# Kernel optimization log

Measured on AMD Instinct MI355X. Metric: run time of the kernel, lower is better.

The kernel has to match this reference:

```python
import jax, jax.numpy as jnp
import numpy as np

B, T, DIM = 2, 2048, 1024
N_HEADS, HEAD_DIM, WINDOW = 16, 64, 512
EPS = 0.01


def _rmsnorm(x, gamma, eps):
    # x: [B, T, H*D] float32; normalize over last dim
    rms = jnp.sqrt(jnp.mean(jnp.square(x), axis=-1, keepdims=True) + eps)
    return x / rms * gamma


def setup_inputs() -> dict:
    key = jax.random.key(0)
    ks = jax.random.split(key, 5)
    s = 1.0 / np.sqrt(DIM)
    return {
        "x": jax.random.normal(ks[0], (B, T, DIM), jnp.float32),
        "wq": jax.random.normal(ks[1], (N_HEADS * HEAD_DIM, DIM), jnp.float32) * s,
        "wk": jax.random.normal(ks[2], (N_HEADS * HEAD_DIM, DIM), jnp.float32) * s,
        "wv": jax.random.normal(ks[3], (N_HEADS * HEAD_DIM, DIM), jnp.float32) * s,
        "wo": jax.random.normal(ks[4], (DIM, N_HEADS * HEAD_DIM), jnp.float32) * s,
        "q_gamma": jnp.ones((N_HEADS * HEAD_DIM,), jnp.float32),
        "k_gamma": jnp.ones((N_HEADS * HEAD_DIM,), jnp.float32),
    }


def reference(x, wq, wk, wv, wo, q_gamma, k_gamma):
    Bx, Tx, _ = x.shape
    H, D = N_HEADS, HEAD_DIM
    # projections (Linear with weight [out,in]): [B,T,H*D]
    q = x @ wq.T
    k = x @ wk.T
    v = (x @ wv.T).reshape(Bx, Tx, H, D).transpose(0, 2, 1, 3)  # [B,H,T,D]
    # QK RMSNorm over the flattened H*D dimension (float32 math)
    q = _rmsnorm(q, q_gamma, 1e-6).reshape(Bx, Tx, H, D).transpose(0, 2, 1, 3)
    k = _rmsnorm(k, k_gamma, 1e-6).reshape(Bx, Tx, H, D).transpose(0, 2, 1, 3)
    scale = 1.0 / np.sqrt(D)
    scores = jnp.einsum("bhqd,bhkd->bhqk", q, k) * scale  # [B,H,T,T]
    # ALiBi bias: slopes[h] * (j - i)
    slopes = jnp.asarray([2.0 ** (-8.0 / H * (h + 1)) for h in range(H)], jnp.float32)
    pos = jnp.arange(Tx)
    dist = (pos[None, :] - pos[:, None]).astype(jnp.float32)  # [T,T], dist[i,j]=j-i
    scores = scores + slopes[None, :, None, None] * dist[None, None]
    # causal (j>i) OR beyond sliding window (i-j > window_size)
    j_minus_i = pos[None, :] - pos[:, None]
    mask = (j_minus_i > 0) | (j_minus_i < -WINDOW)
    scores = jnp.where(mask[None, None], -1e9, scores)
    attn = jax.nn.softmax(scores, axis=-1)
    out = jnp.einsum("bhqk,bhkd->bhqd", attn, v)  # [B,H,T,D]
    out = out.transpose(0, 2, 1, 3).reshape(Bx, Tx, H * D)
    return out @ wo.T
```

## Files before the change

### kernel.cpp

```cpp
#include <hip/hip_runtime.h>
#include <stdint.h>

typedef unsigned short u16;
typedef __bf16 bf16x8 __attribute__((ext_vector_type(8)));
typedef float f32x4 __attribute__((ext_vector_type(4)));

#define MFMA16(a, b, c) __builtin_amdgcn_mfma_f32_16x16x32_bf16((a), (b), (c), 0, 0, 0)

__device__ __forceinline__ u16 f2bf(float f) {
  union { float f; uint32_t u; } v; v.f = f;
  uint32_t r = v.u + 0x7fffu + ((v.u >> 16) & 1u);
  return (u16)(r >> 16);
}
__device__ __forceinline__ float bf2f(u16 h) {
  union { uint32_t u; float f; } v; v.u = ((uint32_t)h) << 16;
  return v.f;
}
__device__ __forceinline__ void gload_lds16(const void* g, void* l) {
  __builtin_amdgcn_global_load_lds(
      (const __attribute__((address_space(1))) uint32_t*)(uintptr_t)g,
      (__attribute__((address_space(3))) uint32_t*)(uintptr_t)l, 16, 0, 0);
}
__device__ __forceinline__ uint32_t cvt_pk_bf16(float a, float b) {
  uint32_t r;
  asm("v_cvt_pk_bf16_f32 %0, %1, %2" : "=v"(r) : "v"(a), "v"(b));
  return r;
}

__global__ void k_cvt_all(const float* __restrict__ x, const float* __restrict__ wq,
                          const float* __restrict__ wk, const float* __restrict__ wv,
                          const float* __restrict__ wo, u16* __restrict__ xb,
                          u16* __restrict__ wqb, u16* __restrict__ wkb, u16* __restrict__ wvb,
                          u16* __restrict__ wob) {
  const int i = blockIdx.x * 256 + threadIdx.x;
  const float* src; u16* dst; int off;
  if (i < 1048576)      { src = x;  dst = xb;  off = i; }
  else if (i < 1310720) { src = wq; dst = wqb; off = i - 1048576; }
  else if (i < 1572864) { src = wk; dst = wkb; off = i - 1310720; }
  else if (i < 1835008) { src = wv; dst = wvb; off = i - 1572864; }
  else                  { src = wo; dst = wob; off = i - 1835008; }
  const float4 v = ((const float4*)src)[off];
  u16 o[4] = { f2bf(v.x), f2bf(v.y), f2bf(v.z), f2bf(v.w) };
  *(uint2*)(dst + 4 * (size_t)off) = *(const uint2*)o;
}

template <bool BF16_OUT>
__device__ __forceinline__ void gemm_core(const u16* __restrict__ A, const u16* __restrict__ Bw,
                                          void* __restrict__ C) {
  constexpr int K = 1024, N = 1024, NT = K / 32;
  __shared__ __align__(16) u16 As[2][128 * 32];
  __shared__ __align__(16) u16 Bs[2][128 * 32];
  const int tid = threadIdx.x, l = tid & 63, w = tid >> 6;
  const int wm = (w >> 1) * 64, wn = (w & 1) * 64;
  const int tn = blockIdx.x * 128, tm = blockIdx.y * 128;
  const int lo = l & 15, hi8 = (l >> 4) * 8;
  f32x4 acc[4][4] = {};

  const int srow = l >> 2, scol = (l & 3) * 8;
  const int c0 = w * 2, c1 = w * 2 + 1;
  const u16* Ag0 = A + (size_t)(tm + c0 * 16 + srow) * K + scol;
  const u16* Ag1 = A + (size_t)(tm + c1 * 16 + srow) * K + scol;
  const u16* Bg0 = Bw + (size_t)(tn + c0 * 16 + srow) * K + scol;
  const u16* Bg1 = Bw + (size_t)(tn + c1 * 16 + srow) * K + scol;

#define STAGE_G(t, buf)                           \
  {                                               \
    const int kt_ = (t) * 32;                     \
    gload_lds16(Ag0 + kt_, &As[(buf)][c0 * 512]); \
    gload_lds16(Ag1 + kt_, &As[(buf)][c1 * 512]); \
    gload_lds16(Bg0 + kt_, &Bs[(buf)][c0 * 512]); \
    gload_lds16(Bg1 + kt_, &Bs[(buf)][c1 * 512]); \
  }

  STAGE_G(0, 0);
  STAGE_G(1, 1);

  for (int t = 0; t < NT; ++t) {
    const int cur = t & 1;
    if (t + 1 < NT) {
      asm volatile("s_waitcnt vmcnt(4)");
    } else {
      asm volatile("s_waitcnt vmcnt(0)");
    }
    __builtin_amdgcn_s_barrier();
    __builtin_amdgcn_sched_barrier(0);

    bf16x8 af[4], bfr[4];
#pragma unroll
    for (int m = 0; m < 4; ++m) af[m] = *(const bf16x8*)&As[cur][(wm + m * 16 + lo) * 32 + hi8];
#pragma unroll
    for (int n = 0; n < 4; ++n) bfr[n] = *(const bf16x8*)&Bs[cur][(wn + n * 16 + lo) * 32 + hi8];
#pragma unroll
    for (int m = 0; m < 4; ++m)
#pragma unroll
      for (int n = 0; n < 4; ++n) acc[m][n] = MFMA16(af[m], bfr[n], acc[m][n]);

    __builtin_amdgcn_sched_barrier(0);
    __builtin_amdgcn_s_barrier();
    __builtin_amdgcn_sched_barrier(0);
    if (t + 2 < NT) STAGE_G(t + 2, cur);
  }
#undef STAGE_G

  const int r0 = (l >> 4) * 4;
#pragma unroll
  for (int m = 0; m < 4; ++m)
#pragma unroll
    for (int n = 0; n < 4; ++n)
#pragma unroll
      for (int r = 0; r < 4; ++r) {
        const size_t idx = (size_t)(tm + wm + m * 16 + r0 + r) * N + (tn + wn + n * 16 + lo);
        if (BF16_OUT) ((u16*)C)[idx] = f2bf(acc[m][n][r]);
        else ((float*)C)[idx] = acc[m][n][r];
      }
}

__global__ __launch_bounds__(256, 3) void k_gemm_qkv(
    const u16* __restrict__ X, const u16* __restrict__ Wq, const u16* __restrict__ Wk,
    const u16* __restrict__ Wv, u16* __restrict__ Q, u16* __restrict__ Kt, u16* __restrict__ V) {
  const u16* B = blockIdx.z == 0 ? Wq : blockIdx.z == 1 ? Wk : Wv;
  u16* C = blockIdx.z == 0 ? Q : blockIdx.z == 1 ? Kt : V;
  gemm_core<true>(X, B, C);
}
__global__ __launch_bounds__(256, 3) void k_gemm_out(const u16* __restrict__ Ao,
                                                     const u16* __restrict__ Wo,
                                                     float* __restrict__ C) {
  gemm_core<false>(Ao, Wo, C);
}

__global__ __launch_bounds__(256) void k_rmsnorm(u16* __restrict__ Q, u16* __restrict__ Kt,
                                                 const float* __restrict__ qg,
                                                 const float* __restrict__ kg) {
  const int row = blockIdx.x;
  u16* base = (row < 4096) ? (Q + (size_t)row * 1024) : (Kt + (size_t)(row - 4096) * 1024);
  const float* g = (row < 4096) ? qg : kg;
  const int tid = threadIdx.x;
  ushort4 v = ((const ushort4*)base)[tid];
  float f0 = bf2f(v.x), f1 = bf2f(v.y), f2 = bf2f(v.z), f3 = bf2f(v.w);
  float ss = f0 * f0 + f1 * f1 + f2 * f2 + f3 * f3;
#pragma unroll
  for (int off = 32; off >= 1; off >>= 1) ss += __shfl_xor(ss, off, 64);
  __shared__ float wsum[4];
  if ((tid & 63) == 0) wsum[tid >> 6] = ss;
  __syncthreads();
  ss = wsum[0] + wsum[1] + wsum[2] + wsum[3];
  const float rinv = rsqrtf(ss * (1.0f / 1024.0f) + 1e-6f);
  const float4 gv = ((const float4*)g)[tid];
  v.x = f2bf(f0 * rinv * gv.x);
  v.y = f2bf(f1 * rinv * gv.y);
  v.z = f2bf(f2 * rinv * gv.z);
  v.w = f2bf(f3 * rinv * gv.w);
  ((ushort4*)base)[tid] = v;
}

__global__ __launch_bounds__(512, 4) void k_attn(const u16* __restrict__ Q,
                                                 const u16* __restrict__ Kt,
                                                 const u16* __restrict__ V,
                                                 u16* __restrict__ O) {
  constexpr int T = 2048, HD = 1024, WIN = 512;
  const int nlin = blockIdx.x + (blockIdx.y << 4) + (blockIdx.z << 8);
  const int wid = (nlin & 7) * 64 + (nlin >> 3);
  const int qb = (wid & 15) * 128, h = (wid >> 4) & 15, b = wid >> 8;
  const int tid = threadIdx.x, l = tid & 63, w = tid >> 6;
  const int lo = l & 15, hi = l >> 4;
  const int qw = qb + w * 16;
  const int qg = qw + lo;

  __shared__ __align__(16) u16 Ks[2][64 * 64];
  __shared__ __align__(16) u16 Vt[2][64 * 72];

  const size_t bT = (size_t)b * T;

  bf16x8 qf[2];
  {
    const u16* Qr = Q + (bT + qw + lo) * HD + h * 64 + hi * 8;
    qf[0] = *(const bf16x8*)(Qr);
    qf[1] = *(const bf16x8*)(Qr + 32);
  }

  const int srow = tid >> 3;
  const int kcol = 8 * ((tid & 7) ^ (srow & 7));
  const int vkv = 2 * (l & 31) + (l >> 5);
  const int vd0 = w * 8;
  const u16* Kg0 = Kt + bT * HD + h * 64;
  const u16* Vg0 = V + bT * HD + h * 64;

  float m_r = -1e30f, l_r = 0.f;
  f32x4 o_acc[4] = {};

  const float L2E = 1.4426950408889634f;
  const float scaleL = 0.125f * L2E;
  const float slopeL = exp2f(-0.5f * (float)(h + 1)) * L2E;
  float cn[4], cr[4];
#pragma unroll
  for (int n = 0; n < 4; ++n) cn[n] = slopeL * (float)(n * 16);
#pragma unroll
  for (int r = 0; r < 4; ++r) cr[r] = slopeL * (float)r;

  const int kvs = (qb >= WIN) ? (qb - WIN) : 0;
  const int nt = (qb + 128 - kvs) >> 6;

  {
    const uint4 pkt = *(const uint4*)(Vg0 + (size_t)(kvs + vkv) * HD + vd0);
    gload_lds16(Kg0 + (size_t)(kvs + srow) * HD + kcol, &Ks[0][tid * 8]);
    const u16* e = (const u16*)&pkt;
#pragma unroll
    for (int j = 0; j < 8; ++j) Vt[0][(vd0 + j) * 72 + vkv] = e[j];
  }
  asm volatile("s_waitcnt vmcnt(0)");
  asm volatile("s_waitcnt lgkmcnt(0)");
  __builtin_amdgcn_s_barrier();
  __builtin_amdgcn_sched_barrier(0);

  for (int t = 0; t < nt; ++t) {
    const int kv0 = kvs + t * 64, cur = t & 1;
    const bool pf_next = (t + 1 < nt);
    uint4 vnext;
    if (pf_next) {
      vnext = *(const uint4*)(Vg0 + (size_t)(kv0 + 64 + vkv) * HD + vd0);
      gload_lds16(Kg0 + (size_t)(kv0 + 64 + srow) * HD + kcol, &Ks[cur ^ 1][tid * 8]);
      asm volatile("s_waitcnt vmcnt(2)");
    } else {
      asm volatile("s_waitcnt vmcnt(0)");
    }
    __builtin_amdgcn_s_barrier();
    __builtin_amdgcn_sched_barrier(0);

    const bool active = (kv0 <= qw + 15) && (kv0 + 63 + WIN >= qw);
    if (active) {
      f32x4 st[4];
      __builtin_amdgcn_s_setprio(1);
#pragma unroll
      for (int n = 0; n < 4; ++n) {
        f32x4 z = {0.f, 0.f, 0.f, 0.f};
        const int row = n * 16 + lo;
        const int swz = (row & 7) << 4;
#pragma unroll
        for (int kk = 0; kk < 2; ++kk) {
          const bf16x8 kf =
              *(const bf16x8*)((const char*)Ks[cur] + row * 128 + ((kk * 64 + hi * 16) ^ swz));
          z = MFMA16(kf, qf[kk], z);
        }
        st[n] = z;
      }
      __builtin_amdgcn_s_setprio(0);

      const int ddb = kv0 + hi * 4 - qg;
      const float bb = slopeL * (float)ddb;
      float bn[4];
#pragma unroll
      for (int n = 0; n < 4; ++n) bn[n] = bb + cn[n];
      const bool interior = (kv0 + 63 <= qw) && (qw + 15 - kv0 <= WIN);
      if (interior) {
#pragma unroll
        for (int n = 0; n < 4; ++n)
#pragma unroll
          for (int r = 0; r < 4; ++r) st[n][r] = st[n][r] * scaleL + (bn[n] + cr[r]);
      } else {
#pragma unroll
        for (int n = 0; n < 4; ++n)
#pragma unroll
          for (int r = 0; r < 4; ++r) {
            const int dd = ddb + n * 16 + r;
            const float s_ = st[n][r] * scaleL + (bn[n] + cr[r]);
            st[n][r] = (dd > 0 || dd < -WIN) ? -1e30f : s_;
          }
      }

      float mx = -1e30f;
#pragma unroll
      for (int n = 0; n < 4; ++n) {
        const float a = fmaxf(st[n][0], st[n][1]), c = fmaxf(st[n][2], st[n][3]);
        mx = fmaxf(mx, fmaxf(a, c));
      }
      mx = fmaxf(mx, __shfl_xor(mx, 16, 64));
      mx = fmaxf(mx, __shfl_xor(mx, 32, 64));
      const float mn = fmaxf(m_r, mx);
      const float alpha = exp2f(m_r - mn);
      m_r = mn;

      float rs = 0.f;
#pragma unroll
      for (int n = 0; n < 4; ++n)
#pragma unroll
        for (int r = 0; r < 4; ++r) {
          const float p = exp2f(st[n][r] - mn);
          st[n][r] = p;
          rs += p;
        }
      rs += __shfl_xor(rs, 16, 64);
      rs += __shfl_xor(rs, 32, 64);
      l_r = l_r * alpha + rs;
#pragma unroll
      for (int nd = 0; nd < 4; ++nd)
#pragma unroll
        for (int r = 0; r < 4; ++r) o_acc[nd][r] *= alpha;

      uint32_t pk[4][2];
#pragma unroll
      for (int n = 0; n < 4; ++n)
#pragma unroll
        for (int d = 0; d < 2; ++d) pk[n][d] = cvt_pk_bf16(st[n][2 * d], st[n][2 * d + 1]);

      uint32_t pfr[2][4];
#pragma unroll
      for (int kk = 0; kk < 2; ++kk)
#pragma unroll
        for (int d = 0; d < 2; ++d) {
          auto s1 = __builtin_amdgcn_permlane32_swap(pk[kk * 2][d], pk[kk * 2 + 1][d], false, false);
          auto s2 = __builtin_amdgcn_permlane16_swap(s1[0], s1[1], false, false);
          pfr[kk][d] = s2[0];
          pfr[kk][2 + d] = s2[1];
        }

      __builtin_amdgcn_s_setprio(1);
#pragma unroll
      for (int kk = 0; kk < 2; ++kk) {
        union { uint32_t u[4]; bf16x8 v; } pu;
#pragma unroll
        for (int d2 = 0; d2 < 4; ++d2) pu.u[d2] = pfr[kk][d2];
        const bf16x8 pv = pu.v;
#pragma unroll
        for (int nd = 0; nd < 4; ++nd) {
          const bf16x8 vf = *(const bf16x8*)&Vt[cur][(nd * 16 + lo) * 72 + kk * 32 + hi * 8];
          o_acc[nd] = MFMA16(vf, pv, o_acc[nd]);
        }
      }
      __builtin_amdgcn_s_setprio(0);
    }

    if (pf_next) {
      const u16* e = (const u16*)&vnext;
#pragma unroll
      for (int j = 0; j < 8; ++j) Vt[cur ^ 1][(vd0 + j) * 72 + vkv] = e[j];
    }
    __builtin_amdgcn_sched_barrier(0);
    asm volatile("s_waitcnt lgkmcnt(0)");
    __builtin_amdgcn_s_barrier();
    __builtin_amdgcn_sched_barrier(0);
  }

  const float inv = 1.f / l_r;
  u16* Og = O + (bT + qw + lo) * HD + h * 64;
#pragma unroll
  for (int nd = 0; nd < 4; ++nd) {
    uint2 pack;
    pack.x = cvt_pk_bf16(o_acc[nd][0] * inv, o_acc[nd][1] * inv);
    pack.y = cvt_pk_bf16(o_acc[nd][2] * inv, o_acc[nd][3] * inv);
    *(uint2*)(Og + nd * 16 + hi * 4) = pack;
  }
}

extern "C" void kernel_launch(void* const* d_in, const int* in_sizes, int n_in,
                              void* d_out, int out_size, void* d_ws, size_t ws_size,
                              hipStream_t stream) {
  const float* x = (const float*)d_in[0];
  const float* wq = (const float*)d_in[1];
  const float* wk = (const float*)d_in[2];
  const float* wv = (const float*)d_in[3];
  const float* wo = (const float*)d_in[4];
  const float* qg = (const float*)d_in[5];
  const float* kg = (const float*)d_in[6];
  float* out = (float*)d_out;

  char* ws = (char*)d_ws;
  const size_t MB = (size_t)1 << 20;
  u16* xb  = (u16*)(ws + 0 * MB);
  u16* wqb = (u16*)(ws + 8 * MB);
  u16* wkb = (u16*)(ws + 10 * MB);
  u16* wvb = (u16*)(ws + 12 * MB);
  u16* wob = (u16*)(ws + 14 * MB);
  u16* qb  = (u16*)(ws + 16 * MB);
  u16* kb  = (u16*)(ws + 24 * MB);
  u16* vb  = (u16*)(ws + 32 * MB);
  u16* ab  = xb;

  k_cvt_all<<<8192, 256, 0, stream>>>(x, wq, wk, wv, wo, xb, wqb, wkb, wvb, wob);
  k_gemm_qkv<<<dim3(8, 32, 3), 256, 0, stream>>>(xb, wqb, wkb, wvb, qb, kb, vb);
  k_rmsnorm<<<8192, 256, 0, stream>>>(qb, kb, qg, kg);
  k_attn<<<dim3(16, 16, 2), 512, 0, stream>>>(qb, kb, vb, ab);
  k_gemm_out<<<dim3(8, 32, 1), 256, 0, stream>>>(ab, wob, out);
}
```

Before: 106.3 us.

## Process 128-key tiles per attention iteration with single-buffered transposed V

Doubles the KV tile from 64 to 128 keys per loop iteration, halving the number of iterations and barrier pairs and the online-softmax rescale overhead. K stays double-buffered via async global-to-LDS loads. V becomes a single LDS buffer written after a barrier, with the global V loads issued early into registers. This adds register pressure (st[8], pk[8][2]) and means more masked work on window edges, and the V stage now waits on all outstanding loads at the end of each iteration, which may expose latency.

```diff
diff --git a/kernel.cpp b/kernel.cpp
--- a/kernel.cpp
+++ b/kernel.cpp
@@ -166,8 +166,8 @@
   const int qw = qb + w * 16;
   const int qg = qw + lo;
 
-  __shared__ __align__(16) u16 Ks[2][64 * 64];
-  __shared__ __align__(16) u16 Vt[2][64 * 72];
+  __shared__ __align__(16) u16 Ks[2][128 * 64];
+  __shared__ __align__(16) u16 Vt[64 * 136];
 
   const size_t bT = (size_t)b * T;
 
@@ -191,47 +191,50 @@
   const float L2E = 1.4426950408889634f;
   const float scaleL = 0.125f * L2E;
   const float slopeL = exp2f(-0.5f * (float)(h + 1)) * L2E;
-  float cn[4], cr[4];
-#pragma unroll
-  for (int n = 0; n < 4; ++n) cn[n] = slopeL * (float)(n * 16);
+  float cn[8], cr[4];
+#pragma unroll
+  for (int n = 0; n < 8; ++n) cn[n] = slopeL * (float)(n * 16);
 #pragma unroll
   for (int r = 0; r < 4; ++r) cr[r] = slopeL * (float)r;
 
   const int kvs = (qb >= WIN) ? (qb - WIN) : 0;
-  const int nt = (qb + 128 - kvs) >> 6;
+  const int nt = (qb + 128 - kvs) >> 7;
 
   {
-    const uint4 pkt = *(const uint4*)(Vg0 + (size_t)(kvs + vkv) * HD + vd0);
     gload_lds16(Kg0 + (size_t)(kvs + srow) * HD + kcol, &Ks[0][tid * 8]);
-    const u16* e = (const u16*)&pkt;
-#pragma unroll
-    for (int j = 0; j < 8; ++j) Vt[0][(vd0 + j) * 72 + vkv] = e[j];
-  }
-  asm volatile("s_waitcnt vmcnt(0)");
+    gload_lds16(Kg0 + (size_t)(kvs + 64 + srow) * HD + kcol, &Ks[0][64 * 64 + tid * 8]);
+    const uint4 p0 = *(const uint4*)(Vg0 + (size_t)(kvs + vkv) * HD + vd0);
+    const uint4 p1 = *(const uint4*)(Vg0 + (size_t)(kvs + 64 + vkv) * HD + vd0);
+    asm volatile("s_waitcnt vmcnt(0)");
+    const u16* e0 = (const u16*)&p0;
+    const u16* e1 = (const u16*)&p1;
+#pragma unroll
+    for (int j = 0; j < 8; ++j) {
+      Vt[(vd0 + j) * 136 + vkv] = e0[j];
+      Vt[(vd0 + j) * 136 + 64 + vkv] = e1[j];
+    }
+  }
   asm volatile("s_waitcnt lgkmcnt(0)");
   __builtin_amdgcn_s_barrier();
   __builtin_amdgcn_sched_barrier(0);
 
   for (int t = 0; t < nt; ++t) {
-    const int kv0 = kvs + t * 64, cur = t & 1;
+    const int kv0 = kvs + t * 128, cur = t & 1;
     const bool pf_next = (t + 1 < nt);
-    uint4 vnext;
+    uint4 vn0, vn1;
     if (pf_next) {
-      vnext = *(const uint4*)(Vg0 + (size_t)(kv0 + 64 + vkv) * HD + vd0);
-      gload_lds16(Kg0 + (size_t)(kv0 + 64 + srow) * HD + kcol, &Ks[cur ^ 1][tid * 8]);
-      asm volatile("s_waitcnt vmcnt(2)");
-    } else {
-      asm volatile("s_waitcnt vmcnt(0)");
-    }
-    __builtin_amdgcn_s_barrier();
-    __builtin_amdgcn_sched_barrier(0);
-
-    const bool active = (kv0 <= qw + 15) && (kv0 + 63 + WIN >= qw);
+      gload_lds16(Kg0 + (size_t)(kv0 + 128 + srow) * HD + kcol, &Ks[cur ^ 1][tid * 8]);
+      gload_lds16(Kg0 + (size_t)(kv0 + 192 + srow) * HD + kcol, &Ks[cur ^ 1][64 * 64 + tid * 8]);
+      vn0 = *(const uint4*)(Vg0 + (size_t)(kv0 + 128 + vkv) * HD + vd0);
+      vn1 = *(const uint4*)(Vg0 + (size_t)(kv0 + 192 + vkv) * HD + vd0);
+    }
+
+    const bool active = (kv0 <= qw + 15) && (kv0 + 127 + WIN >= qw);
     if (active) {
-      f32x4 st[4];
+      f32x4 st[8];
       __builtin_amdgcn_s_setprio(1);
 #pragma unroll
-      for (int n = 0; n < 4; ++n) {
+      for (int n = 0; n < 8; ++n) {
         f32x4 z = {0.f, 0.f, 0.f, 0.f};
         const int row = n * 16 + lo;
         const int swz = (row & 7) << 4;
@@ -247,18 +250,18 @@
 
       const int ddb = kv0 + hi * 4 - qg;
       const float bb = slopeL * (float)ddb;
-      float bn[4];
-#pragma unroll
-      for (int n = 0; n < 4; ++n) bn[n] = bb + cn[n];
-      const bool interior = (kv0 + 63 <= qw) && (qw + 15 - kv0 <= WIN);
+      float bn[8];
+#pragma unroll
+      for (int n = 0; n < 8; ++n) bn[n] = bb + cn[n];
+      const bool interior = (kv0 + 127 <= qw) && (qw + 15 - kv0 <= WIN);
       if (interior) {
 #pragma unroll
-        for (int n = 0; n < 4; ++n)
+        for (int n = 0; n < 8; ++n)
 #pragma unroll
           for (int r = 0; r < 4; ++r) st[n][r] = st[n][r] * scaleL + (bn[n] + cr[r]);
       } else {
 #pragma unroll
-        for (int n = 0; n < 4; ++n)
+        for (int n = 0; n < 8; ++n)
 #pragma unroll
           for (int r = 0; r < 4; ++r) {
             const int dd = ddb + n * 16 + r;
@@ -269,7 +272,7 @@
 
       float mx = -1e30f;
 #pragma unroll
-      for (int n = 0; n < 4; ++n) {
+      for (int n = 0; n < 8; ++n) {
         const float a = fmaxf(st[n][0], st[n][1]), c = fmaxf(st[n][2], st[n][3]);
         mx = fmaxf(mx, fmaxf(a, c));
       }
@@ -281,7 +284,7 @@
 
       float rs = 0.f;
 #pragma unroll
-      for (int n = 0; n < 4; ++n)
+      for (int n = 0; n < 8; ++n)
 #pragma unroll
         for (int r = 0; r < 4; ++r) {
           const float p = exp2f(st[n][r] - mn);
@@ -296,15 +299,15 @@
 #pragma unroll
         for (int r = 0; r < 4; ++r) o_acc[nd][r] *= alpha;
 
-      uint32_t pk[4][2];
-#pragma unroll
-      for (int n = 0; n < 4; ++n)
+      uint32_t pk[8][2];
+#pragma unroll
+      for (int n = 0; n < 8; ++n)
 #pragma unroll
         for (int d = 0; d < 2; ++d) pk[n][d] = cvt_pk_bf16(st[n][2 * d], st[n][2 * d + 1]);
 
-      uint32_t pfr[2][4];
-#pragma unroll
-      for (int kk = 0; kk < 2; ++kk)
+      uint32_t pfr[4][4];
+#pragma unroll
+      for (int kk = 0; kk < 4; ++kk)
 #pragma unroll
         for (int d = 0; d < 2; ++d) {
           auto s1 = __builtin_amdgcn_permlane32_swap(pk[kk * 2][d], pk[kk * 2 + 1][d], false, false);
@@ -315,27 +318,34 @@
 
       __builtin_amdgcn_s_setprio(1);
 #pragma unroll
-      for (int kk = 0; kk < 2; ++kk) {
+      for (int kk = 0; kk < 4; ++kk) {
         union { uint32_t u[4]; bf16x8 v; } pu;
 #pragma unroll
         for (int d2 = 0; d2 < 4; ++d2) pu.u[d2] = pfr[kk][d2];
         const bf16x8 pv = pu.v;
 #pragma unroll
         for (int nd = 0; nd < 4; ++nd) {
-          const bf16x8 vf = *(const bf16x8*)&Vt[cur][(nd * 16 + lo) * 72 + kk * 32 + hi * 8];
+          const bf16x8 vf = *(const bf16x8*)&Vt[(nd * 16 + lo) * 136 + kk * 32 + hi * 8];
           o_acc[nd] = MFMA16(vf, pv, o_acc[nd]);
         }
       }
       __builtin_amdgcn_s_setprio(0);
     }
 
+    __builtin_amdgcn_sched_barrier(0);
+    __builtin_amdgcn_s_barrier();
+    __builtin_amdgcn_sched_barrier(0);
     if (pf_next) {
-      const u16* e = (const u16*)&vnext;
-#pragma unroll
-      for (int j = 0; j < 8; ++j) Vt[cur ^ 1][(vd0 + j) * 72 + vkv] = e[j];
-    }
-    __builtin_amdgcn_sched_barrier(0);
-    asm volatile("s_waitcnt lgkmcnt(0)");
+      asm volatile("s_waitcnt vmcnt(0)");
+      const u16* e0 = (const u16*)&vn0;
+      const u16* e1 = (const u16*)&vn1;
+#pragma unroll
+      for (int j = 0; j < 8; ++j) {
+        Vt[(vd0 + j) * 136 + vkv] = e0[j];
+        Vt[(vd0 + j) * 136 + 64 + vkv] = e1[j];
+      }
+      asm volatile("s_waitcnt lgkmcnt(0)");
+    }
     __builtin_amdgcn_s_barrier();
     __builtin_amdgcn_sched_barrier(0);
   }
```

After: 113.3 us. +6.6%, slower.
